# Performance work log

Measured on AMD Instinct MI355X. Metric: run time of the kernel, lower is better.

Reference implementation:

```python
import jax, jax.numpy as jnp
import numpy as np

B, N, E, K, H = 4, 2048, 512, 16, 8
EMB = 2 * E  # MultiheadAttention embed_dim = input_enc * 2


def setup_inputs() -> dict:
    key = jax.random.key(0)
    ks = jax.random.split(key, 6)
    s = 0.02
    return {
        "x": jax.random.normal(ks[0], (B, N, E), jnp.float32),
        "x_enc": jax.random.normal(ks[1], (B, N, EMB), jnp.float32),
        "w_in": jax.random.normal(ks[2], (3 * EMB, EMB), jnp.float32) * s,
        "b_in": jnp.zeros((3 * EMB,), jnp.float32),
        "w_out": jax.random.normal(ks[3], (EMB, EMB), jnp.float32) * s,
        "b_out": jnp.zeros((EMB,), jnp.float32),
        "k": K,
    }


def _knn_mean(x, k):
    # x: (B, N, E). torch code transposes to (B, E, N) and treats the E channel
    # rows as the 'points' for kNN (distance matrix is (B, E, E)).
    xt = jnp.swapaxes(x, 1, 2)                      # (B, E, N)
    sq = jnp.sum(xt * xt, axis=-1)                  # (B, E)
    dist = sq[:, :, None] + sq[:, None, :] - 2.0 * jnp.einsum("ben,bfn->bef", xt, xt)
    idx = jax.lax.top_k(-dist, k)[1]                # (B, E, k) smallest distances
    # fused gather + mean: avoid the (B, E, E, N) expand from the torch code
    nbrs = jnp.take_along_axis(xt[:, None, :, :], idx[:, :, :, None], axis=2)  # (B, E, k, N)
    return jnp.swapaxes(jnp.mean(nbrs, axis=2), 1, 2)  # (B, N, E)


def _mha(q, kv, w_in, b_in, w_out, b_out, h):
    # faithful torch nn.MultiheadAttention (batch_first) forward
    wq, wk, wv = jnp.split(w_in, 3, axis=0)
    bq, bk, bv = jnp.split(b_in, 3, axis=0)
    Q = q @ wq.T + bq
    Kt = kv @ wk.T + bk
    V = kv @ wv.T + bv
    b, l, emb = Q.shape
    m = Kt.shape[1]
    d = emb // h

    def split_heads(t):
        return t.reshape(t.shape[0], t.shape[1], h, d).transpose(0, 2, 1, 3)

    Qh, Kh, Vh = split_heads(Q), split_heads(Kt), split_heads(V)
    scores = jnp.einsum("bhld,bhmd->bhlm", Qh, Kh) / jnp.sqrt(jnp.float32(d))
    att = jax.nn.softmax(scores, axis=-1)
    o = jnp.einsum("bhlm,bhmd->bhld", att, Vh)      # (B, H, L, d)
    o = o.transpose(0, 2, 1, 3).reshape(b, l, emb)
    return o @ w_out.T + b_out


def reference(x, x_enc, w_in, b_in, w_out, b_out, k):
    b, n, e = x.shape
    x_knn = _knn_mean(x, k)                          # (B, N, E)
    cat = jnp.concatenate([jnp.swapaxes(x, 1, 2), jnp.swapaxes(x_knn, 1, 2)], axis=-1)  # (B, E, 2N)
    # faithful to torch .view(-1, 2*E, N): row-interleaving reshape, NOT a transpose
    q = jnp.swapaxes(cat.reshape(b, 2 * e, n), 1, 2)  # (B, N, 2E)
    attn = _mha(q, x_enc, w_in, b_in, w_out, b_out, H)  # (B, N, 2E)
    return jnp.concatenate([q, attn], axis=1)         # (B, 2N, 2E)
```

## Files before the change

kernel.cpp:

```cpp
#include <hip/hip_runtime.h>
#include <hip/hip_bf16.h>

#define B_ 4
#define N_ 2048
#define E_ 512
#define EMB_ 1024
#define H_ 8
#define D_ 128
#define KNN_ 16

typedef short short8_t __attribute__((ext_vector_type(8)));
typedef short short4_t __attribute__((ext_vector_type(4)));
typedef float float4_t __attribute__((ext_vector_type(4)));

__device__ __forceinline__ short f2bf(float f) {
  unsigned u = __float_as_uint(f);
  unsigned r = u + 0x7fffu + ((u >> 16) & 1u);
  return (short)(r >> 16);
}

__global__ __launch_bounds__(256) void k_sqnp_part(const float* __restrict__ x,
                                                   float* __restrict__ part) {
  const int t = blockIdx.x * 256 + threadIdx.x;
  if (t >= B_ * E_ * 16) return;
  const int be = t & (B_ * E_ - 1), blk = t >> 11;
  const int b = be >> 9, e = be & (E_ - 1);
  const float* p = x + (size_t)b * N_ * E_ + (size_t)blk * 128 * E_ + e;
  float lane[16];
#pragma unroll
  for (int l = 0; l < 16; l++) {
    float pr[8];
#pragma unroll
    for (int j = 0; j < 8; j++) {
      float v = p[(size_t)(j * 16 + l) * E_];
      pr[j] = __fmul_rn(v, v);
    }
    float s01 = __fadd_rn(pr[0], pr[1]);
    float s23 = __fadd_rn(pr[2], pr[3]);
    float s45 = __fadd_rn(pr[4], pr[5]);
    float s67 = __fadd_rn(pr[6], pr[7]);
    lane[l] = __fadd_rn(__fadd_rn(s01, s23), __fadd_rn(s45, s67));
  }
  float bb[8];
#pragma unroll
  for (int l = 0; l < 8; l++) bb[l] = __fadd_rn(lane[l], lane[l + 8]);
  float cc[4];
#pragma unroll
  for (int l = 0; l < 4; l++) cc[l] = __fadd_rn(bb[l], bb[l + 4]);
  part[(size_t)be * 16 + blk] =
      __fadd_rn(__fadd_rn(cc[0], cc[1]), __fadd_rn(cc[2], cc[3]));
}

__global__ __launch_bounds__(256) void k_sqnp_fin(const float* __restrict__ part,
                                                  float* __restrict__ sq) {
  const int t = blockIdx.x * 256 + threadIdx.x;
  if (t >= B_ * E_) return;
  const float* bs = part + (size_t)t * 16;
  float t1[8], t2[4];
#pragma unroll
  for (int l = 0; l < 8; l++) t1[l] = __fadd_rn(bs[2 * l], bs[2 * l + 1]);
#pragma unroll
  for (int l = 0; l < 4; l++) t2[l] = __fadd_rn(t1[2 * l], t1[2 * l + 1]);
  sq[t] = __fadd_rn(__fadd_rn(t2[0], t2[1]), __fadd_rn(t2[2], t2[3]));
}

__global__ __launch_bounds__(256) void k_gram_sym(const float* __restrict__ x,
                                                  float* __restrict__ g) {
  __shared__ float xs[32][36];
  __shared__ float ys[32][36];
  int p = blockIdx.x;
  const int b = blockIdx.y;
  int ti = 0;
  while (p >= 16 - ti) { p -= 16 - ti; ti++; }
  const int tj = ti + p;
  const int i0 = ti * 32, j0 = tj * 32;
  const int tid = threadIdx.x;
  const int li = tid & 15, lj = tid >> 4;
  const int snn = tid >> 3, sc4 = (tid & 7) * 4;
  const float* xb = x + (size_t)b * N_ * E_;

  float a00 = 0.f, a01 = 0.f, a10 = 0.f, a11 = 0.f;
  float4 px = *(const float4*)(xb + (size_t)snn * E_ + i0 + sc4);
  float4 py = *(const float4*)(xb + (size_t)snn * E_ + j0 + sc4);

  for (int n0 = 0; n0 < N_; n0 += 32) {
    __syncthreads();
    *(float4*)&xs[snn][sc4] = px;
    *(float4*)&ys[snn][sc4] = py;
    __syncthreads();
    if (n0 + 32 < N_) {
      px = *(const float4*)(xb + (size_t)(n0 + 32 + snn) * E_ + i0 + sc4);
      py = *(const float4*)(xb + (size_t)(n0 + 32 + snn) * E_ + j0 + sc4);
    }
#pragma unroll
    for (int nn = 0; nn < 32; nn++) {
      const float2 va = *(const float2*)&xs[nn][li * 2];
      const float2 vb = *(const float2*)&ys[nn][lj * 2];
      a00 = __fadd_rn(a00, __fmul_rn(va.x, vb.x));
      a01 = __fadd_rn(a01, __fmul_rn(va.x, vb.y));
      a10 = __fadd_rn(a10, __fmul_rn(va.y, vb.x));
      a11 = __fadd_rn(a11, __fmul_rn(va.y, vb.y));
    }
  }
  float* gb = g + (size_t)b * E_ * E_;
  const int i = i0 + li * 2, j = j0 + lj * 2;
  gb[(size_t)i * E_ + j]           = a00;
  gb[(size_t)i * E_ + j + 1]       = a01;
  gb[(size_t)(i + 1) * E_ + j]     = a10;
  gb[(size_t)(i + 1) * E_ + j + 1] = a11;
  if (ti != tj) {
    gb[(size_t)j * E_ + i]           = a00;
    gb[(size_t)(j + 1) * E_ + i]     = a01;
    gb[(size_t)j * E_ + i + 1]       = a10;
    gb[(size_t)(j + 1) * E_ + i + 1] = a11;
  }
}

__global__ __launch_bounds__(256) void k_topk(const float* __restrict__ sq,
                                              const float* __restrict__ g,
                                              int* __restrict__ idxout) {
  const int bi = blockIdx.x;
  const int b = bi >> 9, i = bi & (E_ - 1);
  const int tid = threadIdx.x;
  const float* gb = g + ((size_t)b * E_ + i) * E_;
  const float* sqb = sq + ((size_t)b << 9);
  __shared__ float val[E_];
  __shared__ float rv[256];
  __shared__ int ri[256];
  const float sqi = sqb[i];
  for (int j = tid; j < E_; j += 256) {
    val[j] = __fsub_rn(__fadd_rn(sqi, sqb[j]), __fmul_rn(2.0f, gb[j]));
  }
  __syncthreads();
  for (int t = 0; t < KNN_; t++) {
    float best = 3.0e38f; int bidx = E_;
    for (int j = tid; j < E_; j += 256) {
      float v = val[j];
      if (v < best) { best = v; bidx = j; }
    }
    rv[tid] = best; ri[tid] = bidx;
    __syncthreads();
    for (int s = 128; s > 0; s >>= 1) {
      if (tid < s) {
        float v2 = rv[tid + s]; int i2 = ri[tid + s];
        if (v2 < rv[tid] || (v2 == rv[tid] && i2 < ri[tid])) {
          rv[tid] = v2; ri[tid] = i2;
        }
      }
      __syncthreads();
    }
    if (tid == 0) {
      idxout[(size_t)bi * KNN_ + t] = ri[0];
      val[ri[0]] = 3.0e38f;
    }
    __syncthreads();
  }
}

__global__ __launch_bounds__(256) void k_knnmean(const float* __restrict__ x,
                                                 const int* __restrict__ idx,
                                                 float* __restrict__ out) {
  const int n = blockIdx.x, b = blockIdx.y;
  const int tid = threadIdx.x;
  __shared__ float xrow[E_];
  const float* xr = x + ((size_t)b * N_ + n) * E_;
  for (int i = tid; i < E_; i += 256) xrow[i] = xr[i];
  __syncthreads();
  float* orow = out + ((size_t)b * (2 * N_) + n) * EMB_;
  for (int i = tid; i < E_; i += 256) {
    const int* id = idx + ((size_t)b * E_ + i) * KNN_;
    float s = 0.f;
#pragma unroll
    for (int t = 0; t < KNN_; t++) s = __fadd_rn(s, xrow[id[t]]);
    float2 w; w.x = xrow[i]; w.y = s * (1.0f / 16.0f);
    *(float2*)&orow[2 * i] = w;
  }
}

__global__ __launch_bounds__(256) void k_cvt(const float* __restrict__ src,
                                             short* __restrict__ dst, int n8) {
  const int t = blockIdx.x * 256 + threadIdx.x;
  if (t >= n8) return;
  const float* s = src + (size_t)t * 8;
  float4 a = *(const float4*)s, b = *(const float4*)(s + 4);
  short8_t v;
  v[0] = f2bf(a.x); v[1] = f2bf(a.y); v[2] = f2bf(a.z); v[3] = f2bf(a.w);
  v[4] = f2bf(b.x); v[5] = f2bf(b.y); v[6] = f2bf(b.z); v[7] = f2bf(b.w);
  *(short8_t*)(dst + (size_t)t * 8) = v;
}

__global__ __launch_bounds__(256) void k_cvt_q(const float* __restrict__ outq,
                                               short* __restrict__ dst) {
  const int t = blockIdx.x * 256 + threadIdx.x;
  const int row = t >> 7, c = (t & 127) * 8;
  const int b = row >> 11, n = row & (N_ - 1);
  const float* s = outq + ((size_t)b * 2 * N_ + n) * EMB_ + c;
  float4 a = *(const float4*)s, bb = *(const float4*)(s + 4);
  short8_t v;
  v[0] = f2bf(a.x);  v[1] = f2bf(a.y);  v[2] = f2bf(a.z);  v[3] = f2bf(a.w);
  v[4] = f2bf(bb.x); v[5] = f2bf(bb.y); v[6] = f2bf(bb.z); v[7] = f2bf(bb.w);
  *(short8_t*)(dst + (size_t)row * EMB_ + c) = v;
}

template<int MODE>
__global__ __launch_bounds__(256) void k_gemm_bf16(
    const short* __restrict__ X, const short* __restrict__ W,
    const float* __restrict__ bias, short* __restrict__ Yb,
    float* __restrict__ Yf) {
  __shared__ __align__(16) short As[128 * 64];
  __shared__ __align__(16) short Bs[128 * 64];
  const int tid = threadIdx.x;
  const int row0 = blockIdx.x * 128, col0 = blockIdx.y * 128;
  const int l = tid & 63, lg = l >> 4, lq = l & 15;
  const int w = tid >> 6, wm = w >> 1, wn = w & 1;
  float4_t acc[4][4];
#pragma unroll
  for (int i = 0; i < 4; i++)
#pragma unroll
    for (int j = 0; j < 4; j++) {
      acc[i][j][0] = 0.f; acc[i][j][1] = 0.f; acc[i][j][2] = 0.f; acc[i][j][3] = 0.f;
    }

  int rr_[4], cc_[4];
#pragma unroll
  for (int ii = 0; ii < 4; ii++) {
    const int cid = ii * 256 + tid;
    rr_[ii] = cid >> 3; cc_[ii] = cid & 7;
  }
  short8_t ar[4], br[4];
#pragma unroll
  for (int ii = 0; ii < 4; ii++) {
    ar[ii] = *(const short8_t*)(X + (size_t)(row0 + rr_[ii]) * EMB_ + cc_[ii] * 8);
    br[ii] = *(const short8_t*)(W + (size_t)(col0 + rr_[ii]) * EMB_ + cc_[ii] * 8);
  }

  for (int kt = 0; kt < 16; kt++) {
    __syncthreads();
#pragma unroll
    for (int ii = 0; ii < 4; ii++) {
      const int idx = rr_[ii] * 64 + ((cc_[ii] * 8) ^ ((rr_[ii] & 7) << 3));
      *(short8_t*)&As[idx] = ar[ii];
      *(short8_t*)&Bs[idx] = br[ii];
    }
    __syncthreads();
    if (kt < 15) {
#pragma unroll
      for (int ii = 0; ii < 4; ii++) {
        ar[ii] = *(const short8_t*)(X + (size_t)(row0 + rr_[ii]) * EMB_ + (kt + 1) * 64 + cc_[ii] * 8);
        br[ii] = *(const short8_t*)(W + (size_t)(col0 + rr_[ii]) * EMB_ + (kt + 1) * 64 + cc_[ii] * 8);
      }
    }
#pragma unroll
    for (int kk = 0; kk < 2; kk++) {
      short8_t af[4], bf[4];
#pragma unroll
      for (int mi = 0; mi < 4; mi++) {
        const int r = wm * 64 + mi * 16 + lq;
        af[mi] = *(const short8_t*)&As[r * 64 + ((kk * 32 + lg * 8) ^ ((r & 7) << 3))];
      }
#pragma unroll
      for (int ni = 0; ni < 4; ni++) {
        const int r = wn * 64 + ni * 16 + lq;
        bf[ni] = *(const short8_t*)&Bs[r * 64 + ((kk * 32 + lg * 8) ^ ((r & 7) << 3))];
      }
#pragma unroll
      for (int mi = 0; mi < 4; mi++)
#pragma unroll
        for (int ni = 0; ni < 4; ni++)
          acc[mi][ni] = __builtin_amdgcn_mfma_f32_16x16x32_bf16(af[mi], bf[ni], acc[mi][ni], 0, 0, 0);
    }
  }
#pragma unroll
  for (int ni = 0; ni < 4; ni++) {
    const int col = col0 + wn * 64 + ni * 16 + lq;
    const float bv = bias[col];
#pragma unroll
    for (int mi = 0; mi < 4; mi++) {
#pragma unroll
      for (int j = 0; j < 4; j++) {
        const int m = row0 + wm * 64 + mi * 16 + lg * 4 + j;
        const float v = acc[mi][ni][j] + bv;
        if (MODE == 0) {
          Yb[(size_t)m * EMB_ + col] = f2bf(v);
        } else if (MODE == 1) {
          const int b2 = m >> 11, n2 = m & (N_ - 1);
          Yf[((size_t)b2 * 2 * N_ + N_ + n2) * EMB_ + col] = v;
        } else {
          const int b2 = m >> 11, n2 = m & (N_ - 1);
          Yb[((size_t)b2 * EMB_ + col) * N_ + n2] = f2bf(v);
        }
      }
    }
  }
}

__global__ __launch_bounds__(256) void k_flash_bf16(
    const short* __restrict__ Qg, const short* __restrict__ Kg,
    const short* __restrict__ Vtg, short* __restrict__ Og) {
  __shared__ __align__(16) short Ks[64 * 128];
  __shared__ __align__(16) short Vs[128 * 64];
  __shared__ __align__(16) short Ps[4][16 * 64];
  const int tid = threadIdx.x;
  const int w = tid >> 6, l = tid & 63, lg = l >> 4, lq = l & 15;
  const int bid = blockIdx.x;
  const int bh = (bid & 7) * 4 + ((bid >> 3) >> 5);
  const int rt = (bid >> 3) & 31;
  const int b = bh >> 3, h = bh & 7;
  const float scale = 0.08838834764831845f;
  const size_t bhoff = (size_t)b * N_ * EMB_ + (size_t)h * D_;
  const int qsw = (lq & 7) << 3;

  short8_t qf[4];
  {
    const short* qrow = Qg + bhoff + (size_t)(rt * 64 + w * 16 + lq) * EMB_;
#pragma unroll
    for (int kk = 0; kk < 4; kk++)
      qf[kk] = *(const short8_t*)(qrow + kk * 32 + lg * 8);
  }
  float4_t oacc[8];
#pragma unroll
  for (int mc = 0; mc < 8; mc++) {
    oacc[mc][0] = 0.f; oacc[mc][1] = 0.f; oacc[mc][2] = 0.f; oacc[mc][3] = 0.f;
  }
  float m = -3.0e38f, lsum = 0.f;

  const short* Vbase = Vtg + (size_t)b * EMB_ * N_ + (size_t)(h * D_) * N_;

  for (int kt = 0; kt < N_ / 64; kt++) {
    __syncthreads();
    const short* Kt = Kg + bhoff + (size_t)(kt * 64) * EMB_;
    const short* Vt = Vbase + kt * 64;
#pragma unroll
    for (int ii = 0; ii < 4; ii++) {
      const int cid = ii * 256 + tid;
      {
        const int r = cid >> 4, c = cid & 15;
        *(short8_t*)&Ks[r * 128 + ((c * 8) ^ ((r & 7) << 3))] =
            *(const short8_t*)(Kt + (size_t)r * EMB_ + c * 8);
      }
      {
        const int r = cid >> 3, c = cid & 7;
        *(short8_t*)&Vs[r * 64 + ((c * 8) ^ ((r & 7) << 3))] =
            *(const short8_t*)(Vt + (size_t)r * N_ + c * 8);
      }
    }
    __syncthreads();

    float4_t sc[4];
#pragma unroll
    for (int c = 0; c < 4; c++) {
      sc[c][0] = 0.f; sc[c][1] = 0.f; sc[c][2] = 0.f; sc[c][3] = 0.f;
      const int krow = c * 16 + lq;
#pragma unroll
      for (int kk = 0; kk < 4; kk++) {
        short8_t kf = *(const short8_t*)&Ks[krow * 128 + ((kk * 32 + lg * 8) ^ qsw)];
        sc[c] = __builtin_amdgcn_mfma_f32_16x16x32_bf16(kf, qf[kk], sc[c], 0, 0, 0);
      }
    }

    float tm = -3.0e38f;
#pragma unroll
    for (int c = 0; c < 4; c++)
#pragma unroll
      for (int j = 0; j < 4; j++) { sc[c][j] *= scale; tm = fmaxf(tm, sc[c][j]); }
    tm = fmaxf(tm, __shfl_xor(tm, 16));
    tm = fmaxf(tm, __shfl_xor(tm, 32));
    const float mn = fmaxf(m, tm);
    const float alpha = __expf(m - mn);
    m = mn;
    float ps = 0.f;
    short4_t pb[4];
#pragma unroll
    for (int c = 0; c < 4; c++) {
#pragma unroll
      for (int j = 0; j < 4; j++) {
        float p = __expf(sc[c][j] - mn);
        ps += p;
        pb[c][j] = f2bf(p);
      }
    }
    ps += __shfl_xor(ps, 16);
    ps += __shfl_xor(ps, 32);
    lsum = lsum * alpha + ps;

#pragma unroll
    for (int c = 0; c < 4; c++)
      *(short4_t*)&Ps[w][lq * 64 + ((c * 16 + lg * 4) ^ qsw)] = pb[c];

#pragma unroll
    for (int mc = 0; mc < 8; mc++) {
      oacc[mc][0] *= alpha; oacc[mc][1] *= alpha;
      oacc[mc][2] *= alpha; oacc[mc][3] *= alpha;
    }
#pragma unroll
    for (int kk = 0; kk < 2; kk++) {
      short8_t pf = *(const short8_t*)&Ps[w][lq * 64 + ((kk * 32 + lg * 8) ^ qsw)];
#pragma unroll
      for (int mc = 0; mc < 8; mc++) {
        const int dd = mc * 16 + lq;
        short8_t vf = *(const short8_t*)&Vs[dd * 64 + ((kk * 32 + lg * 8) ^ qsw)];
        oacc[mc] = __builtin_amdgcn_mfma_f32_16x16x32_bf16(vf, pf, oacc[mc], 0, 0, 0);
      }
    }
  }

  const float linv = 1.0f / lsum;
  short* orow = Og + bhoff + (size_t)(rt * 64 + w * 16 + lq) * EMB_;
#pragma unroll
  for (int mc = 0; mc < 8; mc++) {
    short4_t o;
    o[0] = f2bf(oacc[mc][0] * linv); o[1] = f2bf(oacc[mc][1] * linv);
    o[2] = f2bf(oacc[mc][2] * linv); o[3] = f2bf(oacc[mc][3] * linv);
    *(short4_t*)&orow[mc * 16 + lg * 4] = o;
  }
}

extern "C" void kernel_launch(void* const* d_in, const int* in_sizes, int n_in,
                              void* d_out, int out_size, void* d_ws, size_t ws_size,
                              hipStream_t stream) {
  const float* x     = (const float*)d_in[0];
  const float* x_enc = (const float*)d_in[1];
  const float* w_in  = (const float*)d_in[2];
  const float* b_in  = (const float*)d_in[3];
  const float* w_out = (const float*)d_in[4];
  const float* b_out = (const float*)d_in[5];
  float* out = (float*)d_out;
  char* wsb = (char*)d_ws;

  const size_t oG    = 0;
  const size_t oSq   = oG + (size_t)B_ * E_ * E_ * 4;
  const size_t oPart = oSq + (size_t)B_ * E_ * 4;
  const size_t oIdx  = oPart + (size_t)B_ * E_ * 16 * 4;
  const size_t oXq   = (oIdx + (size_t)B_ * E_ * KNN_ * 4 + 255) & ~(size_t)255;
  const size_t sB    = (size_t)B_ * N_ * EMB_ * 2;
  const size_t oXe   = oXq + sB;
  const size_t oWin  = oXe + sB;
  const size_t oWo   = oWin + 3ull * EMB_ * EMB_ * 2;
  const size_t oQ    = oWo + (size_t)EMB_ * EMB_ * 2;
  const size_t oK    = oQ + sB;
  const size_t oV    = oK + sB;
  const size_t oO    = oV + sB;
  const size_t need  = oO + sB;

  float* g    = (float*)(wsb + oG);
  float* sqv  = (float*)(wsb + oSq);
  float* part = (float*)(wsb + oPart);
  int*   idx  = (int*)(wsb + oIdx);
  short* Xq   = (short*)(wsb + oXq);
  short* Xe   = (short*)(wsb + oXe);
  short* Win  = (short*)(wsb + oWin);
  short* Wo   = (short*)(wsb + oWo);
  short* Qb   = (short*)(wsb + oQ);
  short* Kb   = (short*)(wsb + oK);
  short* Vb   = (short*)(wsb + oV);
  short* Ob   = (ws_size >= need) ? (short*)(wsb + oO) : Qb;

  k_sqnp_part<<<dim3(B_ * E_ * 16 / 256), 256, 0, stream>>>(x, part);
  k_sqnp_fin<<<dim3(B_ * E_ / 256), 256, 0, stream>>>(part, sqv);
  k_gram_sym<<<dim3(136, B_), 256, 0, stream>>>(x, g);
  k_topk<<<dim3(B_ * E_), 256, 0, stream>>>(sqv, g, idx);
  k_knnmean<<<dim3(N_, B_), 256, 0, stream>>>(x, idx, out);

  k_cvt<<<dim3(4096), 256, 0, stream>>>(x_enc, Xe, B_ * N_ * EMB_ / 8);
  k_cvt<<<dim3(1536), 256, 0, stream>>>(w_in, Win, 3 * EMB_ * EMB_ / 8);
  k_cvt<<<dim3(512), 256, 0, stream>>>(w_out, Wo, EMB_ * EMB_ / 8);
  k_cvt_q<<<dim3(4096), 256, 0, stream>>>(out, Xq);

  k_gemm_bf16<0><<<dim3(64, 8), 256, 0, stream>>>(Xq, Win, b_in, Qb, nullptr);
  k_gemm_bf16<0><<<dim3(64, 8), 256, 0, stream>>>(Xe, Win + (size_t)EMB_ * EMB_,
                                                  b_in + EMB_, Kb, nullptr);
  k_gemm_bf16<2><<<dim3(64, 8), 256, 0, stream>>>(Xe, Win + 2ull * EMB_ * EMB_,
                                                  b_in + 2 * EMB_, Vb, nullptr);

  k_flash_bf16<<<dim3(1024), 256, 0, stream>>>(Qb, Kb, Vb, Ob);

  k_gemm_bf16<1><<<dim3(64, 8), 256, 0, stream>>>(Ob, Wo, b_out, nullptr, out);
}
```

Baseline: 397.2 us.

## Prefetch next K/V tile into registers and streamline flash softmax

The flash attention kernel now loads the next K/V tile into registers while the current tile is computed, then writes it to shared memory after the compute, which hides global load latency. The softmax folds the scale into a base-2 exponent with FMA and packs the bf16 conversion. It also skips rescaling the accumulator unless the running max grows by a threshold, and adds MFMA priority hints and a launch-bounds occupancy hint. The tradeoffs are higher register pressure from the prefetch buffers and a lazy-rescale threshold that relies on fp32 headroom.

After: 395.3 us. No clear change (-0.5%).

```diff
diff --git a/kernel.cpp b/kernel.cpp
--- a/kernel.cpp
+++ b/kernel.cpp
@@ -17,6 +17,16 @@
   unsigned u = __float_as_uint(f);
   unsigned r = u + 0x7fffu + ((u >> 16) & 1u);
   return (short)(r >> 16);
+}
+
+__device__ __forceinline__ unsigned pk2bf(float a, float b) {
+  float2 f; f.x = a; f.y = b;
+  __hip_bfloat162 h = __float22bfloat162_rn(f);
+  return *(unsigned*)&h;
+}
+
+__device__ __forceinline__ float fexp2(float x) {
+  return __builtin_amdgcn_exp2f(x);
 }
 
 __global__ __launch_bounds__(256) void k_sqnp_part(const float* __restrict__ x,
@@ -294,7 +304,7 @@
   }
 }
 
-__global__ __launch_bounds__(256) void k_flash_bf16(
+__global__ __launch_bounds__(256, 4) void k_flash_bf16(
     const short* __restrict__ Qg, const short* __restrict__ Kg,
     const short* __restrict__ Vtg, short* __restrict__ Og) {
   __shared__ __align__(16) short Ks[64 * 128];
@@ -306,9 +316,23 @@
   const int bh = (bid & 7) * 4 + ((bid >> 3) >> 5);
   const int rt = (bid >> 3) & 31;
   const int b = bh >> 3, h = bh & 7;
-  const float scale = 0.08838834764831845f;
+  const float c1 = 0.08838834764831845f * 1.4426950408889634f;
   const size_t bhoff = (size_t)b * N_ * EMB_ + (size_t)h * D_;
   const int qsw = (lq & 7) << 3;
+
+  int koff[4], vofs[4], klds[4], vlds[4];
+#pragma unroll
+  for (int ii = 0; ii < 4; ii++) {
+    const int cid = ii * 256 + tid;
+    const int kr = cid >> 4, kc = cid & 15;
+    const int vr = cid >> 3, vc = cid & 7;
+    koff[ii] = kr * EMB_ + kc * 8;
+    vofs[ii] = vr * N_ + vc * 8;
+    klds[ii] = kr * 128 + ((kc * 8) ^ ((kr & 7) << 3));
+    vlds[ii] = vr * 64 + ((vc * 8) ^ ((vr & 7) << 3));
+  }
+  const short* Kt0 = Kg + bhoff;
+  const short* Vt0 = Vtg + (size_t)b * EMB_ * N_ + (size_t)(h * D_) * N_;
 
   short8_t qf[4];
   {
@@ -324,29 +348,32 @@
   }
   float m = -3.0e38f, lsum = 0.f;
 
-  const short* Vbase = Vtg + (size_t)b * EMB_ * N_ + (size_t)(h * D_) * N_;
+  short8_t kreg[4], vreg[4];
+#pragma unroll
+  for (int ii = 0; ii < 4; ii++) {
+    kreg[ii] = *(const short8_t*)(Kt0 + koff[ii]);
+    vreg[ii] = *(const short8_t*)(Vt0 + vofs[ii]);
+  }
+#pragma unroll
+  for (int ii = 0; ii < 4; ii++) {
+    *(short8_t*)&Ks[klds[ii]] = kreg[ii];
+    *(short8_t*)&Vs[vlds[ii]] = vreg[ii];
+  }
+  __syncthreads();
 
   for (int kt = 0; kt < N_ / 64; kt++) {
-    __syncthreads();
-    const short* Kt = Kg + bhoff + (size_t)(kt * 64) * EMB_;
-    const short* Vt = Vbase + kt * 64;
-#pragma unroll
-    for (int ii = 0; ii < 4; ii++) {
-      const int cid = ii * 256 + tid;
-      {
-        const int r = cid >> 4, c = cid & 15;
-        *(short8_t*)&Ks[r * 128 + ((c * 8) ^ ((r & 7) << 3))] =
-            *(const short8_t*)(Kt + (size_t)r * EMB_ + c * 8);
-      }
-      {
-        const int r = cid >> 3, c = cid & 7;
-        *(short8_t*)&Vs[r * 64 + ((c * 8) ^ ((r & 7) << 3))] =
-            *(const short8_t*)(Vt + (size_t)r * N_ + c * 8);
-      }
-    }
-    __syncthreads();
+    if (kt + 1 < N_ / 64) {
+      const short* Kt = Kt0 + (size_t)((kt + 1) * 64) * EMB_;
+      const short* Vt = Vt0 + (kt + 1) * 64;
+#pragma unroll
+      for (int ii = 0; ii < 4; ii++) {
+        kreg[ii] = *(const short8_t*)(Kt + koff[ii]);
+        vreg[ii] = *(const short8_t*)(Vt + vofs[ii]);
+      }
+    }
 
     float4_t sc[4];
+    __builtin_amdgcn_s_setprio(1);
 #pragma unroll
     for (int c = 0; c < 4; c++) {
       sc[c][0] = 0.f; sc[c][1] = 0.f; sc[c][2] = 0.f; sc[c][3] = 0.f;
@@ -357,41 +384,43 @@
         sc[c] = __builtin_amdgcn_mfma_f32_16x16x32_bf16(kf, qf[kk], sc[c], 0, 0, 0);
       }
     }
-
-    float tm = -3.0e38f;
-#pragma unroll
-    for (int c = 0; c < 4; c++)
-#pragma unroll
-      for (int j = 0; j < 4; j++) { sc[c][j] *= scale; tm = fmaxf(tm, sc[c][j]); }
+    __builtin_amdgcn_s_setprio(0);
+
+    float tm = sc[0][0];
+#pragma unroll
+    for (int c = 0; c < 4; c++) {
+      tm = fmaxf(tm, fmaxf(fmaxf(sc[c][0], sc[c][1]), fmaxf(sc[c][2], sc[c][3])));
+    }
     tm = fmaxf(tm, __shfl_xor(tm, 16));
     tm = fmaxf(tm, __shfl_xor(tm, 32));
-    const float mn = fmaxf(m, tm);
-    const float alpha = __expf(m - mn);
-    m = mn;
+    if (__any(tm > m + 62.7f)) {
+      const float mn = fmaxf(m, tm);
+      const float alpha = fexp2((m - mn) * c1);
+      m = mn;
+      lsum *= alpha;
+#pragma unroll
+      for (int mc = 0; mc < 8; mc++) {
+        oacc[mc][0] *= alpha; oacc[mc][1] *= alpha;
+        oacc[mc][2] *= alpha; oacc[mc][3] *= alpha;
+      }
+    }
+    const float mc1 = m * c1;
     float ps = 0.f;
-    short4_t pb[4];
 #pragma unroll
     for (int c = 0; c < 4; c++) {
-#pragma unroll
-      for (int j = 0; j < 4; j++) {
-        float p = __expf(sc[c][j] - mn);
-        ps += p;
-        pb[c][j] = f2bf(p);
-      }
+      float p0 = fexp2(__builtin_fmaf(sc[c][0], c1, -mc1));
+      float p1 = fexp2(__builtin_fmaf(sc[c][1], c1, -mc1));
+      float p2 = fexp2(__builtin_fmaf(sc[c][2], c1, -mc1));
+      float p3 = fexp2(__builtin_fmaf(sc[c][3], c1, -mc1));
+      ps += (p0 + p1) + (p2 + p3);
+      uint2 pw; pw.x = pk2bf(p0, p1); pw.y = pk2bf(p2, p3);
+      *(uint2*)&Ps[w][lq * 64 + ((c * 16 + lg * 4) ^ qsw)] = pw;
     }
     ps += __shfl_xor(ps, 16);
     ps += __shfl_xor(ps, 32);
-    lsum = lsum * alpha + ps;
-
-#pragma unroll
-    for (int c = 0; c < 4; c++)
-      *(short4_t*)&Ps[w][lq * 64 + ((c * 16 + lg * 4) ^ qsw)] = pb[c];
-
-#pragma unroll
-    for (int mc = 0; mc < 8; mc++) {
-      oacc[mc][0] *= alpha; oacc[mc][1] *= alpha;
-      oacc[mc][2] *= alpha; oacc[mc][3] *= alpha;
-    }
+    lsum += ps;
+
+    __builtin_amdgcn_s_setprio(1);
 #pragma unroll
     for (int kk = 0; kk < 2; kk++) {
       short8_t pf = *(const short8_t*)&Ps[w][lq * 64 + ((kk * 32 + lg * 8) ^ qsw)];
@@ -401,6 +430,17 @@
         short8_t vf = *(const short8_t*)&Vs[dd * 64 + ((kk * 32 + lg * 8) ^ qsw)];
         oacc[mc] = __builtin_amdgcn_mfma_f32_16x16x32_bf16(vf, pf, oacc[mc], 0, 0, 0);
       }
+    }
+    __builtin_amdgcn_s_setprio(0);
+
+    __syncthreads();
+    if (kt + 1 < N_ / 64) {
+#pragma unroll
+      for (int ii = 0; ii < 4; ii++) {
+        *(short8_t*)&Ks[klds[ii]] = kreg[ii];
+        *(short8_t*)&Vs[vlds[ii]] = vreg[ii];
+      }
+      __syncthreads();
     }
   }
 
```
